# Kernel tuning notes

Hardware: AMD Instinct MI355X
Metric: run time of the kernel (lower is better)

Reference implementation:

```python
import jax, jax.numpy as jnp
import numpy as np

N_NODES = 100000


def graph_conv(x, edge_index, w_rel, w_root, b):
    # PyG GraphConv with aggr='add':
    # out_i = W_root @ x_i + W_rel @ (sum_{j in N(i)} x_j) + b
    src, dst = edge_index[0], edge_index[1]
    agg = jax.ops.segment_sum(x[src], dst, num_segments=x.shape[0])  # [N, F_in]
    return x @ w_root.T + agg @ w_rel.T + b


def setup_inputs() -> dict:
    key = jax.random.key(0)
    k = jax.random.split(key, 8)
    c_in, c_hid, c_out = 128, 64, 16
    x = jax.random.normal(k[0], (N_NODES, c_in), dtype=jnp.float32)
    edge_index = jax.random.randint(k[1], (2, 640000), 0, N_NODES, dtype=jnp.int64)
    s1 = 1.0 / np.sqrt(c_in)
    s2 = 1.0 / np.sqrt(c_hid)
    return {
        "x": x,
        "edge_index": edge_index,
        "w1_rel": jax.random.uniform(k[2], (c_hid, c_in), jnp.float32, -s1, s1),
        "w1_root": jax.random.uniform(k[3], (c_hid, c_in), jnp.float32, -s1, s1),
        "b1": jax.random.uniform(k[4], (c_hid,), jnp.float32, -s1, s1),
        "w2_rel": jax.random.uniform(k[5], (c_out, c_hid), jnp.float32, -s2, s2),
        "w2_root": jax.random.uniform(k[6], (c_out, c_hid), jnp.float32, -s2, s2),
        "b2": jax.random.uniform(k[7], (c_out,), jnp.float32, -s2, s2),
    }


def reference(x, edge_index, w1_rel, w1_root, b1, w2_rel, w2_root, b2):
    h = graph_conv(x, edge_index, w1_rel, w1_root, b1)
    h = jax.nn.relu(h)
    # dropout is identity in eval mode (deterministic reference)
    h = graph_conv(h, edge_index, w2_rel, w2_root, b2)
    return jax.nn.log_softmax(h, axis=1)
```

## Files before the change

kernel.cpp:

```cpp
#include <hip/hip_runtime.h>
#include <math.h>

constexpr int CIN = 128, CHID = 64, COUT = 16;

__global__ void detect_kernel(const int* __restrict__ e, int* __restrict__ flag) {
    int v = e[2 * threadIdx.x + 1];
    unsigned long long b = __ballot(v == 0);
    if (threadIdx.x == 0) flag[0] = (b == 0xFFFFFFFFFFFFFFFFULL) ? 1 : 0;
}

__global__ void convert_hist(const int* __restrict__ e, int E,
                             const int* __restrict__ flag,
                             int* __restrict__ srcI, int* __restrict__ dstI,
                             int* __restrict__ counts) {
    int is64 = flag[0];
    int stride = gridDim.x * blockDim.x;
    for (int t = blockIdx.x * blockDim.x + threadIdx.x; t < E; t += stride) {
        int s, d;
        if (is64) { s = e[2 * t]; d = e[2 * (E + t)]; }
        else      { s = e[t];     d = e[E + t];       }
        srcI[t] = s;
        dstI[t] = d;
        atomicAdd(&counts[d], 1);
    }
}

__global__ __launch_bounds__(256)
void scan_partials(const int* __restrict__ counts, int N, int* __restrict__ blocksum) {
    __shared__ int red[256];
    const int tid = threadIdx.x;
    const int base = blockIdx.x * 1024 + tid * 4;
    int s = 0;
#pragma unroll
    for (int i = 0; i < 4; ++i) {
        int idx = base + i;
        if (idx < N) s += counts[idx];
    }
    red[tid] = s;
    __syncthreads();
    for (int d = 128; d > 0; d >>= 1) {
        if (tid < d) red[tid] += red[tid + d];
        __syncthreads();
    }
    if (tid == 0) blocksum[blockIdx.x] = red[0];
}

__global__ __launch_bounds__(1024)
void scan_blocksums(const int* __restrict__ blocksum, int NB, int* __restrict__ blockoff) {
    __shared__ int part[1024];
    const int tid = threadIdx.x;
    part[tid] = (tid < NB) ? blocksum[tid] : 0;
    __syncthreads();
    for (int d = 1; d < 1024; d <<= 1) {
        int v = (tid >= d) ? part[tid - d] : 0;
        __syncthreads();
        part[tid] += v;
        __syncthreads();
    }
    if (tid < NB) blockoff[tid] = (tid == 0) ? 0 : part[tid - 1];
}

__global__ __launch_bounds__(256)
void scan_apply(const int* __restrict__ counts, int N, const int* __restrict__ blockoff,
                int* __restrict__ rowptr, int* __restrict__ cursor) {
    __shared__ int part[256];
    const int tid = threadIdx.x;
    const int base = blockIdx.x * 1024 + tid * 4;
    int c[4];
    int s = 0;
#pragma unroll
    for (int i = 0; i < 4; ++i) {
        int idx = base + i;
        c[i] = (idx < N) ? counts[idx] : 0;
        s += c[i];
    }
    part[tid] = s;
    __syncthreads();
    for (int d = 1; d < 256; d <<= 1) {
        int v = (tid >= d) ? part[tid - d] : 0;
        __syncthreads();
        part[tid] += v;
        __syncthreads();
    }
    int prefix = blockoff[blockIdx.x] + ((tid == 0) ? 0 : part[tid - 1]);
#pragma unroll
    for (int i = 0; i < 4; ++i) {
        int idx = base + i;
        if (idx < N) {
            rowptr[idx] = prefix;
            cursor[idx] = prefix;
            prefix += c[i];
            if (idx == N - 1) rowptr[N] = prefix;
        }
    }
}

__global__ void fill_kernel(const int* __restrict__ srcI, const int* __restrict__ dstI,
                            int E, int* __restrict__ cursor, int* __restrict__ edgesrc) {
    int stride = gridDim.x * blockDim.x;
    for (int t = blockIdx.x * blockDim.x + threadIdx.x; t < E; t += stride) {
        int p = atomicAdd(&cursor[dstI[t]], 1);
        edgesrc[p] = srcI[t];
    }
}

template<int K, int KT, int OA, int OB, int NSLOT, int T>
__global__ __launch_bounds__(512, 6)
void gemm_dual(const float* __restrict__ X, int N,
               const float* __restrict__ Wa, const float* __restrict__ Wb,
               const float* __restrict__ bias,
               float* __restrict__ Da, float* __restrict__ Db) {
    constexpr int O = OA + OB;
    constexpr int OG = O / 4;
    constexpr int TILE = NSLOT * T;
    constexpr int PADKT = KT + 4;
    constexpr int BLOCK = OG * NSLOT;
    static_assert(BLOCK == 512, "block size mismatch");

    __shared__ float wT[KT * O];
    __shared__ float xs[TILE * PADKT];
    const int tid = threadIdx.x;

    const int og = tid % OG;
    const int slot = tid / OG;
    const int o4 = og * 4;
    float4 bv = make_float4(0.f, 0.f, 0.f, 0.f);
    if (o4 < OA) bv = *(const float4*)&bias[o4];

    const int n0 = blockIdx.x * TILE;

    float4 acc[T];
#pragma unroll
    for (int i = 0; i < T; ++i) acc[i] = make_float4(0.f, 0.f, 0.f, 0.f);

    for (int kt = 0; kt < K; kt += KT) {
        for (int i4 = tid; i4 < OA * (KT / 4); i4 += BLOCK) {
            int o = i4 % OA, kq = i4 / OA;
            float4 v = *(const float4*)&Wa[o * K + kt + kq * 4];
            wT[(4 * kq + 0) * O + o] = v.x;
            wT[(4 * kq + 1) * O + o] = v.y;
            wT[(4 * kq + 2) * O + o] = v.z;
            wT[(4 * kq + 3) * O + o] = v.w;
        }
        for (int i4 = tid; i4 < OB * (KT / 4); i4 += BLOCK) {
            int o = i4 % OB, kq = i4 / OB;
            float4 v = *(const float4*)&Wb[o * K + kt + kq * 4];
            wT[(4 * kq + 0) * O + OA + o] = v.x;
            wT[(4 * kq + 1) * O + OA + o] = v.y;
            wT[(4 * kq + 2) * O + OA + o] = v.z;
            wT[(4 * kq + 3) * O + OA + o] = v.w;
        }
        for (int i4 = tid; i4 < TILE * (KT / 4); i4 += BLOCK) {
            int node = i4 / (KT / 4), kq = i4 % (KT / 4);
            int n = n0 + node;
            float4 v = make_float4(0.f, 0.f, 0.f, 0.f);
            if (n < N) v = *(const float4*)&X[(size_t)n * K + kt + kq * 4];
            *(float4*)&xs[node * PADKT + kq * 4] = v;
        }
        __syncthreads();

        const float* xrow = &xs[slot * T * PADKT];
#pragma unroll 2
        for (int kq = 0; kq < KT / 4; ++kq) {
            float4 w0 = *(const float4*)&wT[(4 * kq + 0) * O + o4];
            float4 w1 = *(const float4*)&wT[(4 * kq + 1) * O + o4];
            float4 w2 = *(const float4*)&wT[(4 * kq + 2) * O + o4];
            float4 w3 = *(const float4*)&wT[(4 * kq + 3) * O + o4];
#pragma unroll
            for (int i = 0; i < T; ++i) {
                float4 xq = *(const float4*)&xrow[i * PADKT + kq * 4];
                acc[i].x = fmaf(xq.x, w0.x, acc[i].x);
                acc[i].y = fmaf(xq.x, w0.y, acc[i].y);
                acc[i].z = fmaf(xq.x, w0.z, acc[i].z);
                acc[i].w = fmaf(xq.x, w0.w, acc[i].w);
                acc[i].x = fmaf(xq.y, w1.x, acc[i].x);
                acc[i].y = fmaf(xq.y, w1.y, acc[i].y);
                acc[i].z = fmaf(xq.y, w1.z, acc[i].z);
                acc[i].w = fmaf(xq.y, w1.w, acc[i].w);
                acc[i].x = fmaf(xq.z, w2.x, acc[i].x);
                acc[i].y = fmaf(xq.z, w2.y, acc[i].y);
                acc[i].z = fmaf(xq.z, w2.z, acc[i].z);
                acc[i].w = fmaf(xq.z, w2.w, acc[i].w);
                acc[i].x = fmaf(xq.w, w3.x, acc[i].x);
                acc[i].y = fmaf(xq.w, w3.y, acc[i].y);
                acc[i].z = fmaf(xq.w, w3.z, acc[i].z);
                acc[i].w = fmaf(xq.w, w3.w, acc[i].w);
            }
        }
        __syncthreads();
    }

#pragma unroll
    for (int i = 0; i < T; ++i) {
        int n = n0 + slot * T + i;
        if (n >= N) continue;
        float4 r = acc[i];
        if (o4 < OA) {
            r.x += bv.x; r.y += bv.y; r.z += bv.z; r.w += bv.w;
            *(float4*)&Da[(size_t)n * OA + o4] = r;
        } else {
            *(float4*)&Db[(size_t)n * OB + (o4 - OA)] = r;
        }
    }
}

__global__ void gather_relu64(const int* __restrict__ rowptr, const int* __restrict__ edgesrc,
                              const float* __restrict__ T1, float* __restrict__ A, int N) {
    constexpr int F = 64, Q = F / 4;
    int idx = blockIdx.x * blockDim.x + threadIdx.x;
    int n = idx / Q, q = idx % Q;
    if (n >= N) return;
    int beg = rowptr[n], end = rowptr[n + 1];
    float4 acc0 = make_float4(0.f, 0.f, 0.f, 0.f);
    float4 acc1 = make_float4(0.f, 0.f, 0.f, 0.f);
    int j = beg;
    for (; j + 1 < end; j += 2) {
        int s0 = edgesrc[j];
        int s1 = edgesrc[j + 1];
        float4 v0 = *(const float4*)&T1[(size_t)s0 * F + q * 4];
        float4 v1 = *(const float4*)&T1[(size_t)s1 * F + q * 4];
        acc0.x += v0.x; acc0.y += v0.y; acc0.z += v0.z; acc0.w += v0.w;
        acc1.x += v1.x; acc1.y += v1.y; acc1.z += v1.z; acc1.w += v1.w;
    }
    if (j < end) {
        int s0 = edgesrc[j];
        float4 v0 = *(const float4*)&T1[(size_t)s0 * F + q * 4];
        acc0.x += v0.x; acc0.y += v0.y; acc0.z += v0.z; acc0.w += v0.w;
    }
    acc0.x += acc1.x; acc0.y += acc1.y; acc0.z += acc1.z; acc0.w += acc1.w;
    float4 a = *(const float4*)&A[(size_t)n * F + q * 4];
    a.x = fmaxf(a.x + acc0.x, 0.f);
    a.y = fmaxf(a.y + acc0.y, 0.f);
    a.z = fmaxf(a.z + acc0.z, 0.f);
    a.w = fmaxf(a.w + acc0.w, 0.f);
    *(float4*)&A[(size_t)n * F + q * 4] = a;
}

__global__ void gather_lsm(const int* __restrict__ rowptr, const int* __restrict__ edgesrc,
                           const float* __restrict__ T3, const float* __restrict__ T2,
                           float* __restrict__ out, int N) {
    int idx = blockIdx.x * blockDim.x + threadIdx.x;
    int n = idx / 4, c = idx % 4;
    if (n >= N) return;
    int beg = rowptr[n], end = rowptr[n + 1];
    float4 acc0 = make_float4(0.f, 0.f, 0.f, 0.f);
    float4 acc1 = make_float4(0.f, 0.f, 0.f, 0.f);
    int j = beg;
    for (; j + 1 < end; j += 2) {
        int s0 = edgesrc[j];
        int s1 = edgesrc[j + 1];
        float4 v0 = *(const float4*)&T2[(size_t)s0 * 16 + c * 4];
        float4 v1 = *(const float4*)&T2[(size_t)s1 * 16 + c * 4];
        acc0.x += v0.x; acc0.y += v0.y; acc0.z += v0.z; acc0.w += v0.w;
        acc1.x += v1.x; acc1.y += v1.y; acc1.z += v1.z; acc1.w += v1.w;
    }
    if (j < end) {
        int s0 = edgesrc[j];
        float4 v0 = *(const float4*)&T2[(size_t)s0 * 16 + c * 4];
        acc0.x += v0.x; acc0.y += v0.y; acc0.z += v0.z; acc0.w += v0.w;
    }
    acc0.x += acc1.x; acc0.y += acc1.y; acc0.z += acc1.z; acc0.w += acc1.w;
    float4 t = *(const float4*)&T3[(size_t)n * 16 + c * 4];
    float4 v = make_float4(t.x + acc0.x, t.y + acc0.y, t.z + acc0.z, t.w + acc0.w);
    float m = fmaxf(fmaxf(v.x, v.y), fmaxf(v.z, v.w));
    for (int d = 1; d < 4; d <<= 1) m = fmaxf(m, __shfl_xor(m, d, 4));
    float s = expf(v.x - m) + expf(v.y - m) + expf(v.z - m) + expf(v.w - m);
    for (int d = 1; d < 4; d <<= 1) s += __shfl_xor(s, d, 4);
    float ls = m + logf(s);
    float4 r = make_float4(v.x - ls, v.y - ls, v.z - ls, v.w - ls);
    *(float4*)&out[(size_t)n * 16 + c * 4] = r;
}

extern "C" void kernel_launch(void* const* d_in, const int* in_sizes, int n_in,
                              void* d_out, int out_size, void* d_ws, size_t ws_size,
                              hipStream_t stream) {
    const float* X      = (const float*)d_in[0];
    const int*   EIDX   = (const int*)d_in[1];
    const float* W1REL  = (const float*)d_in[2];
    const float* W1ROOT = (const float*)d_in[3];
    const float* B1     = (const float*)d_in[4];
    const float* W2REL  = (const float*)d_in[5];
    const float* W2ROOT = (const float*)d_in[6];
    const float* B2     = (const float*)d_in[7];
    float* OUT = (float*)d_out;

    const int N = in_sizes[0] / CIN;
    const int E = in_sizes[1] / 2;
    const int NB = (N + 1023) / 1024;

    char* wsb = (char*)d_ws;
    size_t off = 0;
    auto alloc = [&](size_t bytes) { void* p = wsb + off; off += (bytes + 255) & ~size_t(255); return p; };

    int* flag     = (int*)alloc(256);
    int* srcI     = (int*)alloc((size_t)E * 4);
    int* dstI     = (int*)alloc((size_t)E * 4);
    int* edgesrc  = (int*)alloc((size_t)E * 4);
    int* counts   = (int*)alloc((size_t)N * 4);
    int* rowptr   = (int*)alloc((size_t)(N + 1) * 4);
    int* cursor   = (int*)alloc((size_t)N * 4);
    int* blocksum = (int*)alloc((size_t)NB * 4);
    int* blockoff = (int*)alloc((size_t)NB * 4);
    float* A      = (float*)alloc((size_t)N * CHID * 4);
    float* Bt     = (float*)alloc((size_t)N * CHID * 4);
    if (off > ws_size) return;

    float* T3 = Bt;
    float* T2 = Bt + (size_t)N * COUT;

    hipMemsetAsync(counts, 0, (size_t)N * 4, stream);

    detect_kernel<<<1, 64, 0, stream>>>(EIDX, flag);
    convert_hist<<<1024, 256, 0, stream>>>(EIDX, E, flag, srcI, dstI, counts);
    scan_partials<<<NB, 256, 0, stream>>>(counts, N, blocksum);
    scan_blocksums<<<1, 1024, 0, stream>>>(blocksum, NB, blockoff);
    scan_apply<<<NB, 256, 0, stream>>>(counts, N, blockoff, rowptr, cursor);
    fill_kernel<<<1024, 256, 0, stream>>>(srcI, dstI, E, cursor, edgesrc);

    {
        constexpr int TILE = 16 * 4;
        int grid = (N + TILE - 1) / TILE;
        gemm_dual<128, 32, 64, 64, 16, 4><<<grid, 512, 0, stream>>>(X, N, W1ROOT, W1REL, B1, A, Bt);
    }

    {
        int threads = N * 16;
        gather_relu64<<<(threads + 255) / 256, 256, 0, stream>>>(rowptr, edgesrc, Bt, A, N);
    }

    {
        constexpr int TILE = 64 * 2;
        int grid = (N + TILE - 1) / TILE;
        gemm_dual<64, 32, 16, 16, 64, 2><<<grid, 512, 0, stream>>>(A, N, W2ROOT, W2REL, B2, T3, T2);
    }

    {
        int threads = N * 4;
        gather_lsm<<<(threads + 255) / 256, 256, 0, stream>>>(rowptr, edgesrc, T3, T2, OUT, N);
    }
}
```

Baseline: 197.5 us.

## Replace layer-1 dual GEMM with wave-per-output-slice kernel using scalar weight loads

Adds a gemm_wave kernel in which each block stages 64 nodes of X in shared memory. Each of its 8 waves computes 16 output columns for those nodes, one node per lane. Because the wave index is made uniform with readfirstlane, the weight reads become wave-uniform and can be served from scalar/constant loads instead of a shared-memory weight tile. This is meant to cut LDS traffic and synchronisation in the first-layer GEMM, at the cost of more accumulator registers per lane and repeated global weight reads per block.

```diff
diff --git a/kernel.cpp b/kernel.cpp
--- a/kernel.cpp
+++ b/kernel.cpp
@@ -101,6 +101,77 @@
     for (int t = blockIdx.x * blockDim.x + threadIdx.x; t < E; t += stride) {
         int p = atomicAdd(&cursor[dstI[t]], 1);
         edgesrc[p] = srcI[t];
+    }
+}
+
+template<int K, int OH, int WPB>
+__global__ __launch_bounds__(WPB * 64)
+void gemm_wave(const float* __restrict__ X, int N,
+               const float* __restrict__ Wa, const float* __restrict__ Wb,
+               const float* __restrict__ bias,
+               float* __restrict__ Da, float* __restrict__ Db) {
+    constexpr int O  = 2 * OH;
+    constexpr int QW = O / WPB;
+    constexpr int NQ = QW / 4;
+    constexpr int PADK = K + 4;
+    constexpr int NODES = 64;
+
+    __shared__ float xs[NODES * PADK];
+
+    const int tid  = threadIdx.x;
+    const int lane = tid & 63;
+    const int wid  = __builtin_amdgcn_readfirstlane(tid >> 6);
+    const int n0   = blockIdx.x * NODES;
+
+    for (int i4 = tid; i4 < NODES * (K / 4); i4 += WPB * 64) {
+        int node = i4 / (K / 4), kq = i4 % (K / 4);
+        int n = n0 + node;
+        float4 v = make_float4(0.f, 0.f, 0.f, 0.f);
+        if (n < N) v = *(const float4*)&X[(size_t)n * K + kq * 4];
+        *(float4*)&xs[node * PADK + kq * 4] = v;
+    }
+    __syncthreads();
+
+    const int ocomb = wid * QW;
+    const bool isA = (ocomb < OH);
+    const float* Wp = isA ? Wa : Wb;
+    const int ob = isA ? ocomb : (ocomb - OH);
+
+    float acc[QW];
+#pragma unroll
+    for (int o = 0; o < QW; ++o) acc[o] = 0.f;
+
+    const float* xrow = &xs[lane * PADK];
+
+#pragma unroll 4
+    for (int kq = 0; kq < K / 4; ++kq) {
+        float4 xv = *(const float4*)&xrow[kq * 4];
+#pragma unroll
+        for (int o = 0; o < QW; ++o) {
+            const float* wp = &Wp[(size_t)(ob + o) * K + kq * 4];
+            acc[o] = fmaf(xv.x, wp[0], acc[o]);
+            acc[o] = fmaf(xv.y, wp[1], acc[o]);
+            acc[o] = fmaf(xv.z, wp[2], acc[o]);
+            acc[o] = fmaf(xv.w, wp[3], acc[o]);
+        }
+    }
+
+    const int n = n0 + lane;
+    if (n < N) {
+#pragma unroll
+        for (int q = 0; q < NQ; ++q) {
+            float4 r = make_float4(acc[q * 4 + 0], acc[q * 4 + 1],
+                                   acc[q * 4 + 2], acc[q * 4 + 3]);
+            if (isA) {
+                r.x += bias[ob + q * 4 + 0];
+                r.y += bias[ob + q * 4 + 1];
+                r.z += bias[ob + q * 4 + 2];
+                r.w += bias[ob + q * 4 + 3];
+                *(float4*)&Da[(size_t)n * OH + ob + q * 4] = r;
+            } else {
+                *(float4*)&Db[(size_t)n * OH + ob + q * 4] = r;
+            }
+        }
     }
 }
 
@@ -318,9 +389,8 @@
     fill_kernel<<<1024, 256, 0, stream>>>(srcI, dstI, E, cursor, edgesrc);
 
     {
-        constexpr int TILE = 16 * 4;
-        int grid = (N + TILE - 1) / TILE;
-        gemm_dual<128, 32, 64, 64, 16, 4><<<grid, 512, 0, stream>>>(X, N, W1ROOT, W1REL, B1, A, Bt);
+        int grid = (N + 63) / 64;
+        gemm_wave<128, 64, 8><<<grid, 512, 0, stream>>>(X, N, W1ROOT, W1REL, B1, A, Bt);
     }
 
     {
```

Result: slower. 250.1 us (+26.6%).
